# Kernel optimization log

Hardware: AMD Instinct MI355X
Metric: run time of the kernel (lower is better)

Reference implementation:

```python
import jax, jax.numpy as jnp
import numpy as np

D_MODEL = 512
NUM_HEADS = 8
D_K = D_MODEL // NUM_HEADS
B, L = 2, 4096


def setup_inputs() -> dict:
    key = jax.random.key(0)
    ks = jax.random.split(key, 11)
    s = 1.0 / np.sqrt(D_MODEL)
    return {
        "Q": jax.random.normal(ks[0], (B, L, D_MODEL), jnp.float32),
        "K": jax.random.normal(ks[1], (B, L, D_MODEL), jnp.float32),
        "V": jax.random.normal(ks[2], (B, L, D_MODEL), jnp.float32),
        "Wq": jax.random.normal(ks[3], (D_MODEL, D_MODEL), jnp.float32) * s,
        "bq": jax.random.normal(ks[4], (D_MODEL,), jnp.float32) * s,
        "Wk": jax.random.normal(ks[5], (D_MODEL, D_MODEL), jnp.float32) * s,
        "bk": jax.random.normal(ks[6], (D_MODEL,), jnp.float32) * s,
        "Wv": jax.random.normal(ks[7], (D_MODEL, D_MODEL), jnp.float32) * s,
        "bv": jax.random.normal(ks[8], (D_MODEL,), jnp.float32) * s,
        "Wo": jax.random.normal(ks[9], (D_MODEL, D_MODEL), jnp.float32) * s,
        "bo": jax.random.normal(ks[10], (D_MODEL,), jnp.float32) * s,
    }


def reference(Q, K, V, Wq, bq, Wk, bk, Wv, bv, Wo, bo):
    b, l, d = Q.shape
    h, dk = NUM_HEADS, D_K
    # projections: [B, L, D] -> [B, H, L, dk]
    def proj(x, W, bias):
        y = x @ W.T + bias
        return y.reshape(b, l, h, dk).transpose(0, 2, 1, 3)
    q = proj(Q, Wq, bq)
    k = proj(K, Wk, bk)
    v = proj(V, Wv, bv)
    scores = jnp.einsum("bhqd,bhkd->bhqk", q, k) / jnp.sqrt(jnp.float32(dk))
    attn = jax.nn.softmax(scores, axis=-1)
    head_out = jnp.einsum("bhqk,bhkd->bhqd", attn, v)
    out = head_out.transpose(0, 2, 1, 3).reshape(b, l, d)
    return out @ Wo.T + bo
```

## Files before the change

### kernel.cpp

```cpp
#include <hip/hip_runtime.h>
#include <hip/hip_bf16.h>

#define SEQ 4096
#define DM 512
#define DK 64
#define NT (SEQ / 64)

typedef __attribute__((ext_vector_type(8))) short bf16x8;
typedef __attribute__((ext_vector_type(4))) short bf16x4;
typedef __attribute__((ext_vector_type(4))) float f32x4;

#define QSCL 0.18033688011112043f

static __device__ __forceinline__ short bf16h(float f) {
    union { __hip_bfloat16 h; short s; } u;
    u.h = __float2bfloat16(f);
    return u.s;
}

static __device__ __forceinline__ float fexp2(float x) {
#if __has_builtin(__builtin_amdgcn_exp2f)
    return __builtin_amdgcn_exp2f(x);
#else
    return exp2f(x);
#endif
}

static __device__ __forceinline__ void cvt16r(float4 a, float4 b, float4 e, float4 d,
                                              short* dst) {
    bf16x8 x0, x1;
    x0[0] = bf16h(a.x); x0[1] = bf16h(a.y); x0[2] = bf16h(a.z); x0[3] = bf16h(a.w);
    x0[4] = bf16h(b.x); x0[5] = bf16h(b.y); x0[6] = bf16h(b.z); x0[7] = bf16h(b.w);
    x1[0] = bf16h(e.x); x1[1] = bf16h(e.y); x1[2] = bf16h(e.z); x1[3] = bf16h(e.w);
    x1[4] = bf16h(d.x); x1[5] = bf16h(d.y); x1[6] = bf16h(d.z); x1[7] = bf16h(d.w);
    *(bf16x8*)dst = x0;
    *(bf16x8*)(dst + 8) = x1;
}

__global__ __launch_bounds__(512) void proj_qkv(
        const float* __restrict__ Qx, const float* __restrict__ Kx, const float* __restrict__ Vx,
        const float* __restrict__ Wq, const float* __restrict__ Wk, const float* __restrict__ Wv,
        const float* __restrict__ bq, const float* __restrict__ bk, const float* __restrict__ bv,
        short* __restrict__ qo, short* __restrict__ ko, short* __restrict__ vo) {
    __shared__ short lds[2][128][72];
    short (*As)[72] = lds[0];
    short (*Bs)[72] = lds[1];
    const int z = blockIdx.z;
    const float* X    = z == 0 ? Qx : z == 1 ? Kx : Vx;
    const float* W    = z == 0 ? Wq : z == 1 ? Wk : Wv;
    const float* bias = z == 0 ? bq : z == 1 ? bk : bv;

    const int t = threadIdx.x, lane = t & 63, w = t >> 6;
    const int g = lane >> 4, c = lane & 15;
    const int wr = w >> 2, wc = w & 3;
    const int row = t >> 2, sc = t & 3;
    const int m0 = blockIdx.x << 7, n0 = blockIdx.y << 7;

    f32x4 acc[4][2] = {};
    const float* px = X + (size_t)(m0 + row) * DM + sc * 16;
    const float* pw = W + (size_t)(n0 + row) * DM + sc * 16;

    float4 x0 = *(const float4*)px,       x1 = *(const float4*)(px + 4),
           x2 = *(const float4*)(px + 8), x3 = *(const float4*)(px + 12);
    float4 w0 = *(const float4*)pw,       w1 = *(const float4*)(pw + 4),
           w2 = *(const float4*)(pw + 8), w3 = *(const float4*)(pw + 12);

    for (int kt = 0; kt < DM / 64; ++kt) {
        cvt16r(x0, x1, x2, x3, &As[row][sc * 16]);
        cvt16r(w0, w1, w2, w3, &Bs[row][sc * 16]);
        __syncthreads();
        if (kt + 1 < DM / 64) {
            px += 64; pw += 64;
            x0 = *(const float4*)px;       x1 = *(const float4*)(px + 4);
            x2 = *(const float4*)(px + 8); x3 = *(const float4*)(px + 12);
            w0 = *(const float4*)pw;       w1 = *(const float4*)(pw + 4);
            w2 = *(const float4*)(pw + 8); w3 = *(const float4*)(pw + 12);
        }
        #pragma unroll
        for (int kc = 0; kc < 2; ++kc) {
            bf16x8 a8[4], b8[2];
            #pragma unroll
            for (int i = 0; i < 4; ++i)
                a8[i] = *(bf16x8*)&As[wr * 64 + i * 16 + c][kc * 32 + 8 * g];
            #pragma unroll
            for (int j = 0; j < 2; ++j)
                b8[j] = *(bf16x8*)&Bs[wc * 32 + j * 16 + c][kc * 32 + 8 * g];
            #pragma unroll
            for (int i = 0; i < 4; ++i)
                #pragma unroll
                for (int j = 0; j < 2; ++j)
                    acc[i][j] = __builtin_amdgcn_mfma_f32_16x16x32_bf16(a8[i], b8[j], acc[i][j], 0, 0, 0);
        }
        __syncthreads();
    }

    const int b = m0 >> 12;
    if (z != 2) {
        short* Yp = z == 0 ? qo : ko;
        const float scl = z == 0 ? QSCL : 1.0f;
        #pragma unroll
        for (int j = 0; j < 2; ++j) {
            const int n = n0 + wc * 32 + j * 16 + c;
            const float bsj = bias[n];
            const int h = n >> 6, d = n & 63;
            short* base = Yp + ((size_t)(b * 8 + h) * SEQ) * DK + d;
            #pragma unroll
            for (int i = 0; i < 4; ++i)
                #pragma unroll
                for (int r = 0; r < 4; ++r) {
                    const int m = m0 + wr * 64 + i * 16 + 4 * g + r;
                    base[(size_t)(m & 4095) * DK] = bf16h((acc[i][j][r] + bsj) * scl);
                }
        }
    } else {
        short* L = &lds[0][0][0];
        #pragma unroll
        for (int j = 0; j < 2; ++j) {
            const int nl = wc * 32 + j * 16 + c;
            const float bsj = bias[n0 + nl];
            #pragma unroll
            for (int i = 0; i < 4; ++i)
                #pragma unroll
                for (int r = 0; r < 4; ++r)
                    L[nl * 136 + wr * 64 + i * 16 + 4 * g + r] = bf16h(acc[i][j][r] + bsj);
        }
        __syncthreads();
        const int rrow = t >> 2, q = t & 3;
        const int n = n0 + rrow, h = n >> 6, d = n & 63;
        short* dst = vo + ((size_t)(b * 8 + h) * DK + d) * SEQ + (m0 & 4095) + q * 32;
        #pragma unroll
        for (int k = 0; k < 4; ++k)
            *(bf16x8*)(dst + 8 * k) = *(bf16x8*)&L[rrow * 136 + q * 32 + 8 * k];
    }
}

__global__ __launch_bounds__(512) void proj_out(const short* __restrict__ Xb,
        const float* __restrict__ W, const float* __restrict__ bias, float* __restrict__ Y) {
    __shared__ short lds[2][128][72];
    short (*As)[72] = lds[0];
    short (*Bs)[72] = lds[1];
    const int t = threadIdx.x, lane = t & 63, w = t >> 6;
    const int g = lane >> 4, c = lane & 15;
    const int wr = w >> 2, wc = w & 3;
    const int row = t >> 2, sc = t & 3;
    const int m0 = blockIdx.x << 7, n0 = blockIdx.y << 7;

    f32x4 acc[4][2] = {};
    const short* px = Xb + (size_t)(m0 + row) * DM + sc * 16;
    const float* pw = W + (size_t)(n0 + row) * DM + sc * 16;

    bf16x8 xb0 = *(const bf16x8*)px, xb1 = *(const bf16x8*)(px + 8);
    float4 w0 = *(const float4*)pw,       w1 = *(const float4*)(pw + 4),
           w2 = *(const float4*)(pw + 8), w3 = *(const float4*)(pw + 12);

    for (int kt = 0; kt < DM / 64; ++kt) {
        *(bf16x8*)&As[row][sc * 16]     = xb0;
        *(bf16x8*)&As[row][sc * 16 + 8] = xb1;
        cvt16r(w0, w1, w2, w3, &Bs[row][sc * 16]);
        __syncthreads();
        if (kt + 1 < DM / 64) {
            px += 64; pw += 64;
            xb0 = *(const bf16x8*)px; xb1 = *(const bf16x8*)(px + 8);
            w0 = *(const float4*)pw;       w1 = *(const float4*)(pw + 4);
            w2 = *(const float4*)(pw + 8); w3 = *(const float4*)(pw + 12);
        }
        #pragma unroll
        for (int kc = 0; kc < 2; ++kc) {
            bf16x8 a8[4], b8[2];
            #pragma unroll
            for (int i = 0; i < 4; ++i)
                a8[i] = *(bf16x8*)&As[wr * 64 + i * 16 + c][kc * 32 + 8 * g];
            #pragma unroll
            for (int j = 0; j < 2; ++j)
                b8[j] = *(bf16x8*)&Bs[wc * 32 + j * 16 + c][kc * 32 + 8 * g];
            #pragma unroll
            for (int i = 0; i < 4; ++i)
                #pragma unroll
                for (int j = 0; j < 2; ++j)
                    acc[i][j] = __builtin_amdgcn_mfma_f32_16x16x32_bf16(a8[i], b8[j], acc[i][j], 0, 0, 0);
        }
        __syncthreads();
    }

    #pragma unroll
    for (int j = 0; j < 2; ++j) {
        const int n = n0 + wc * 32 + j * 16 + c;
        const float bsj = bias[n];
        #pragma unroll
        for (int i = 0; i < 4; ++i)
            #pragma unroll
            for (int r = 0; r < 4; ++r) {
                const int m = m0 + wr * 64 + i * 16 + 4 * g + r;
                Y[(size_t)m * DM + n] = acc[i][j][r] + bsj;
            }
    }
}

__global__ __launch_bounds__(256) void attn_fwd(const short* __restrict__ qp,
        const short* __restrict__ kp, const short* __restrict__ vtp, short* __restrict__ ho) {
    __shared__ short Ks[64][72];
    __shared__ short Vts[64][76];
    const int t = threadIdx.x, lane = t & 63, w = t >> 6;
    const int g = lane >> 4, c = lane & 15;
    const int sr = t >> 2, sc = t & 3;
    const int q0 = blockIdx.x << 6, bh = blockIdx.y;

    const short* qrow = qp + ((size_t)bh * SEQ + q0 + 16 * w + c) * DK;
    const bf16x8 qf0 = *(const bf16x8*)(qrow + 8 * g);
    const bf16x8 qf1 = *(const bf16x8*)(qrow + 32 + 8 * g);

    f32x4 o4[4] = {};
    float m_run = -3.0e38f, l_run = 0.f;

    const short* kptr = kp + (size_t)bh * SEQ * DK + (size_t)sr * DK + sc * 16;
    const short* vptr = vtp + (size_t)bh * DK * SEQ + (size_t)sr * SEQ + sc * 16;
    bf16x8 kr0 = *(const bf16x8*)kptr;
    bf16x8 kr1 = *(const bf16x8*)(kptr + 8);
    bf16x8 vr0 = *(const bf16x8*)vptr;
    bf16x8 vr1 = *(const bf16x8*)(vptr + 8);

    for (int kt = 0; kt < NT; ++kt) {
        *(bf16x8*)&Ks[sr][sc * 16]     = kr0;
        *(bf16x8*)&Ks[sr][sc * 16 + 8] = kr1;
        {
            bf16x4 t0 = {vr0[0], vr0[1], vr0[2], vr0[3]};
            bf16x4 t1 = {vr0[4], vr0[5], vr0[6], vr0[7]};
            bf16x4 t2 = {vr1[0], vr1[1], vr1[2], vr1[3]};
            bf16x4 t3 = {vr1[4], vr1[5], vr1[6], vr1[7]};
            *(bf16x4*)&Vts[sr][sc * 16]      = t0;
            *(bf16x4*)&Vts[sr][sc * 16 + 4]  = t1;
            *(bf16x4*)&Vts[sr][sc * 16 + 8]  = t2;
            *(bf16x4*)&Vts[sr][sc * 16 + 12] = t3;
        }
        __syncthreads();
        if (kt + 1 < NT) {
            kptr += 64 * DK;
            vptr += 64;
            kr0 = *(const bf16x8*)kptr;
            kr1 = *(const bf16x8*)(kptr + 8);
            vr0 = *(const bf16x8*)vptr;
            vr1 = *(const bf16x8*)(vptr + 8);
        }

        f32x4 s4[4] = {};
        #pragma unroll
        for (int f = 0; f < 4; ++f) {
            bf16x8 a8 = *(bf16x8*)&Ks[16 * f + c][8 * g];
            s4[f] = __builtin_amdgcn_mfma_f32_16x16x32_bf16(a8, qf0, s4[f], 0, 0, 0);
        }
        #pragma unroll
        for (int f = 0; f < 4; ++f) {
            bf16x8 a8 = *(bf16x8*)&Ks[16 * f + c][32 + 8 * g];
            s4[f] = __builtin_amdgcn_mfma_f32_16x16x32_bf16(a8, qf1, s4[f], 0, 0, 0);
        }

        float pm = s4[0][0];
        #pragma unroll
        for (int f = 0; f < 4; ++f) {
            #pragma unroll
            for (int r = 0; r < 4; ++r) pm = fmaxf(pm, s4[f][r]);
        }
        pm = fmaxf(pm, __shfl_xor(pm, 16));
        pm = fmaxf(pm, __shfl_xor(pm, 32));

        if (__any(pm > m_run + 8.0f)) {
            float mnew  = fmaxf(m_run, pm);
            float alpha = fexp2(m_run - mnew);
            l_run *= alpha;
            #pragma unroll
            for (int fd = 0; fd < 4; ++fd) {
                #pragma unroll
                for (int r = 0; r < 4; ++r) o4[fd][r] *= alpha;
            }
            m_run = mnew;
        }

        float rs = 0.f;
        #pragma unroll
        for (int f = 0; f < 4; ++f) {
            #pragma unroll
            for (int r = 0; r < 4; ++r) {
                float p = fexp2(s4[f][r] - m_run);
                s4[f][r] = p;
                rs += p;
            }
        }
        rs += __shfl_xor(rs, 16);
        rs += __shfl_xor(rs, 32);
        l_run += rs;

        #pragma unroll
        for (int f = 0; f < 4; ++f) {
            bf16x4 pb = { bf16h(s4[f][0]), bf16h(s4[f][1]), bf16h(s4[f][2]), bf16h(s4[f][3]) };
            #pragma unroll
            for (int fd = 0; fd < 4; ++fd) {
                bf16x4 va = *(bf16x4*)&Vts[16 * fd + c][16 * f + 4 * g];
                o4[fd] = __builtin_amdgcn_mfma_f32_16x16x16bf16_1k(va, pb, o4[fd], 0, 0, 0);
            }
        }
        __syncthreads();
    }

    const float inv = 1.0f / l_run;
    short (&Ls)[64][72] = Ks;
    #pragma unroll
    for (int fd = 0; fd < 4; ++fd) {
        #pragma unroll
        for (int r = 0; r < 4; ++r)
            Ls[16 * w + c][16 * fd + 4 * g + r] = bf16h(o4[fd][r] * inv);
    }
    __syncthreads();
    const int b = bh >> 3, h = bh & 7;
    bf16x8 r0 = *(bf16x8*)&Ls[sr][sc * 16];
    bf16x8 r1 = *(bf16x8*)&Ls[sr][sc * 16 + 8];
    short* dst = ho + ((size_t)(b * SEQ + q0 + sr)) * DM + h * DK + sc * 16;
    *(bf16x8*)dst = r0;
    *(bf16x8*)(dst + 8) = r1;
}

extern "C" void kernel_launch(void* const* d_in, const int* in_sizes, int n_in,
                              void* d_out, int out_size, void* d_ws, size_t ws_size,
                              hipStream_t stream) {
    const float* Q  = (const float*)d_in[0];
    const float* K  = (const float*)d_in[1];
    const float* V  = (const float*)d_in[2];
    const float* Wq = (const float*)d_in[3];
    const float* bq = (const float*)d_in[4];
    const float* Wk = (const float*)d_in[5];
    const float* bk = (const float*)d_in[6];
    const float* Wv = (const float*)d_in[7];
    const float* bv = (const float*)d_in[8];
    const float* Wo = (const float*)d_in[9];
    const float* bo = (const float*)d_in[10];

    const size_t NIN = (size_t)2 * SEQ * DM;

    short* qws  = (short*)d_ws;
    short* kws  = qws + NIN;
    short* vtws = kws + NIN;
    short* hws  = vtws + NIN;

    proj_qkv<<<dim3(64, 4, 3), 512, 0, stream>>>(Q, K, V, Wq, Wk, Wv, bq, bk, bv,
                                                 qws, kws, vtws);
    attn_fwd<<<dim3(SEQ / 64, 16), 256, 0, stream>>>(qws, kws, vtws, hws);
    proj_out<<<dim3(64, 4), 512, 0, stream>>>(hws, Wo, bo, (float*)d_out);
}
```

Before: 284.2 us.

## Double-buffer K/V tiles in LDS and compute softmax row sums via MFMA

The attention kernel now keeps two LDS buffers for the K and V^T tiles. The next tile is written into the alternate buffer after the current tile's compute, which leaves one barrier per iteration instead of two. The softmax denominator is now accumulated with an extra MFMA against a ones vector, using the bf16-rounded probabilities, instead of per-lane sums plus cross-lane shuffles. The max reduction is also rebalanced into a shallower tree. This doubles LDS use per block, which may reduce occupancy, and changes the normalizer to sum bf16-rounded values.

```diff
diff --git a/kernel.cpp b/kernel.cpp
--- a/kernel.cpp
+++ b/kernel.cpp
@@ -198,8 +198,8 @@
 
 __global__ __launch_bounds__(256) void attn_fwd(const short* __restrict__ qp,
         const short* __restrict__ kp, const short* __restrict__ vtp, short* __restrict__ ho) {
-    __shared__ short Ks[64][72];
-    __shared__ short Vts[64][76];
+    __shared__ short Ks[2][64][72];
+    __shared__ short Vts[2][64][76];
     const int t = threadIdx.x, lane = t & 63, w = t >> 6;
     const int g = lane >> 4, c = lane & 15;
     const int sr = t >> 2, sc = t & 3;
@@ -210,30 +210,36 @@
     const bf16x8 qf1 = *(const bf16x8*)(qrow + 32 + 8 * g);
 
     f32x4 o4[4] = {};
-    float m_run = -3.0e38f, l_run = 0.f;
+    f32x4 l4 = {};
+    float m_run = -3.0e38f;
+    const bf16x4 ones = { (short)0x3F80, (short)0x3F80, (short)0x3F80, (short)0x3F80 };
 
     const short* kptr = kp + (size_t)bh * SEQ * DK + (size_t)sr * DK + sc * 16;
     const short* vptr = vtp + (size_t)bh * DK * SEQ + (size_t)sr * SEQ + sc * 16;
-    bf16x8 kr0 = *(const bf16x8*)kptr;
-    bf16x8 kr1 = *(const bf16x8*)(kptr + 8);
-    bf16x8 vr0 = *(const bf16x8*)vptr;
-    bf16x8 vr1 = *(const bf16x8*)(vptr + 8);
-
+
+    {
+        bf16x8 kr0 = *(const bf16x8*)kptr;
+        bf16x8 kr1 = *(const bf16x8*)(kptr + 8);
+        bf16x8 vr0 = *(const bf16x8*)vptr;
+        bf16x8 vr1 = *(const bf16x8*)(vptr + 8);
+        *(bf16x8*)&Ks[0][sr][sc * 16]     = kr0;
+        *(bf16x8*)&Ks[0][sr][sc * 16 + 8] = kr1;
+        bf16x4 t0 = {vr0[0], vr0[1], vr0[2], vr0[3]};
+        bf16x4 t1 = {vr0[4], vr0[5], vr0[6], vr0[7]};
+        bf16x4 t2 = {vr1[0], vr1[1], vr1[2], vr1[3]};
+        bf16x4 t3 = {vr1[4], vr1[5], vr1[6], vr1[7]};
+        *(bf16x4*)&Vts[0][sr][sc * 16]      = t0;
+        *(bf16x4*)&Vts[0][sr][sc * 16 + 4]  = t1;
+        *(bf16x4*)&Vts[0][sr][sc * 16 + 8]  = t2;
+        *(bf16x4*)&Vts[0][sr][sc * 16 + 12] = t3;
+    }
+    __syncthreads();
+
+    int p = 0;
     for (int kt = 0; kt < NT; ++kt) {
-        *(bf16x8*)&Ks[sr][sc * 16]     = kr0;
-        *(bf16x8*)&Ks[sr][sc * 16 + 8] = kr1;
-        {
-            bf16x4 t0 = {vr0[0], vr0[1], vr0[2], vr0[3]};
-            bf16x4 t1 = {vr0[4], vr0[5], vr0[6], vr0[7]};
-            bf16x4 t2 = {vr1[0], vr1[1], vr1[2], vr1[3]};
-            bf16x4 t3 = {vr1[4], vr1[5], vr1[6], vr1[7]};
-            *(bf16x4*)&Vts[sr][sc * 16]      = t0;
-            *(bf16x4*)&Vts[sr][sc * 16 + 4]  = t1;
-            *(bf16x4*)&Vts[sr][sc * 16 + 8]  = t2;
-            *(bf16x4*)&Vts[sr][sc * 16 + 12] = t3;
-        }
-        __syncthreads();
-        if (kt + 1 < NT) {
+        const bool more = (kt + 1 < NT);
+        bf16x8 kr0, kr1, vr0, vr1;
+        if (more) {
             kptr += 64 * DK;
             vptr += 64;
             kr0 = *(const bf16x8*)kptr;
@@ -245,28 +251,28 @@
         f32x4 s4[4] = {};
         #pragma unroll
         for (int f = 0; f < 4; ++f) {
-            bf16x8 a8 = *(bf16x8*)&Ks[16 * f + c][8 * g];
+            bf16x8 a8 = *(bf16x8*)&Ks[p][16 * f + c][8 * g];
             s4[f] = __builtin_amdgcn_mfma_f32_16x16x32_bf16(a8, qf0, s4[f], 0, 0, 0);
         }
         #pragma unroll
         for (int f = 0; f < 4; ++f) {
-            bf16x8 a8 = *(bf16x8*)&Ks[16 * f + c][32 + 8 * g];
+            bf16x8 a8 = *(bf16x8*)&Ks[p][16 * f + c][32 + 8 * g];
             s4[f] = __builtin_amdgcn_mfma_f32_16x16x32_bf16(a8, qf1, s4[f], 0, 0, 0);
         }
 
-        float pm = s4[0][0];
-        #pragma unroll
-        for (int f = 0; f < 4; ++f) {
-            #pragma unroll
-            for (int r = 0; r < 4; ++r) pm = fmaxf(pm, s4[f][r]);
-        }
+        float a0 = fmaxf(fmaxf(s4[0][0], s4[0][1]), s4[0][2]);
+        float a1 = fmaxf(fmaxf(s4[0][3], s4[1][0]), s4[1][1]);
+        float a2 = fmaxf(fmaxf(s4[1][2], s4[1][3]), s4[2][0]);
+        float a3 = fmaxf(fmaxf(s4[2][1], s4[2][2]), s4[2][3]);
+        float a4 = fmaxf(fmaxf(s4[3][0], s4[3][1]), s4[3][2]);
+        float pm = fmaxf(fmaxf(fmaxf(a0, a1), a2), fmaxf(fmaxf(a3, a4), s4[3][3]));
         pm = fmaxf(pm, __shfl_xor(pm, 16));
         pm = fmaxf(pm, __shfl_xor(pm, 32));
 
         if (__any(pm > m_run + 8.0f)) {
             float mnew  = fmaxf(m_run, pm);
             float alpha = fexp2(m_run - mnew);
-            l_run *= alpha;
+            l4[0] *= alpha; l4[1] *= alpha; l4[2] *= alpha; l4[3] *= alpha;
             #pragma unroll
             for (int fd = 0; fd < 4; ++fd) {
                 #pragma unroll
@@ -275,34 +281,43 @@
             m_run = mnew;
         }
 
-        float rs = 0.f;
         #pragma unroll
         for (int f = 0; f < 4; ++f) {
             #pragma unroll
-            for (int r = 0; r < 4; ++r) {
-                float p = fexp2(s4[f][r] - m_run);
-                s4[f][r] = p;
-                rs += p;
-            }
-        }
-        rs += __shfl_xor(rs, 16);
-        rs += __shfl_xor(rs, 32);
-        l_run += rs;
+            for (int r = 0; r < 4; ++r)
+                s4[f][r] = fexp2(s4[f][r] - m_run);
+        }
 
         #pragma unroll
         for (int f = 0; f < 4; ++f) {
             bf16x4 pb = { bf16h(s4[f][0]), bf16h(s4[f][1]), bf16h(s4[f][2]), bf16h(s4[f][3]) };
+            l4 = __builtin_amdgcn_mfma_f32_16x16x16bf16_1k(ones, pb, l4, 0, 0, 0);
             #pragma unroll
             for (int fd = 0; fd < 4; ++fd) {
-                bf16x4 va = *(bf16x4*)&Vts[16 * fd + c][16 * f + 4 * g];
+                bf16x4 va = *(bf16x4*)&Vts[p][16 * fd + c][16 * f + 4 * g];
                 o4[fd] = __builtin_amdgcn_mfma_f32_16x16x16bf16_1k(va, pb, o4[fd], 0, 0, 0);
             }
         }
-        __syncthreads();
-    }
-
-    const float inv = 1.0f / l_run;
-    short (&Ls)[64][72] = Ks;
+
+        if (more) {
+            const int q2 = p ^ 1;
+            *(bf16x8*)&Ks[q2][sr][sc * 16]     = kr0;
+            *(bf16x8*)&Ks[q2][sr][sc * 16 + 8] = kr1;
+            bf16x4 t0 = {vr0[0], vr0[1], vr0[2], vr0[3]};
+            bf16x4 t1 = {vr0[4], vr0[5], vr0[6], vr0[7]};
+            bf16x4 t2 = {vr1[0], vr1[1], vr1[2], vr1[3]};
+            bf16x4 t3 = {vr1[4], vr1[5], vr1[6], vr1[7]};
+            *(bf16x4*)&Vts[q2][sr][sc * 16]      = t0;
+            *(bf16x4*)&Vts[q2][sr][sc * 16 + 4]  = t1;
+            *(bf16x4*)&Vts[q2][sr][sc * 16 + 8]  = t2;
+            *(bf16x4*)&Vts[q2][sr][sc * 16 + 12] = t3;
+        }
+        __syncthreads();
+        p ^= 1;
+    }
+
+    const float inv = 1.0f / l4[0];
+    short (*Ls)[72] = Ks[0];
     #pragma unroll
     for (int fd = 0; fd < 4; ++fd) {
         #pragma unroll
```

Result: no change. 283.8 us (-0.1%).
